# Performance work log

Hardware: AMD Instinct MI355X
Metric: run time of the kernel (lower is better)

## Reference

```python
import jax, jax.numpy as jnp
import numpy as np

N_NODES = 50000
N_EDGES = 800000
IN_DIM = 232
EMB = 300
HID = 2 * EMB
N_LAYERS = 5
BN_EPS = 1e-5


def setup_inputs() -> dict:
    key = jax.random.key(0)
    ks = jax.random.split(key, 12)
    x = jax.random.normal(ks[0], (N_NODES, IN_DIM), dtype=jnp.float32)
    edge_index = jax.random.randint(ks[1], (2, N_EDGES), 0, N_NODES, dtype=jnp.int64)
    edge_attr = jax.random.normal(ks[2], (N_EDGES, 9), dtype=jnp.float32)
    s_in = 1.0 / np.sqrt(IN_DIM)
    s_emb = 1.0 / np.sqrt(EMB)
    s_hid = 1.0 / np.sqrt(HID)
    lin_in_w = jax.random.uniform(ks[3], (IN_DIM, EMB), jnp.float32, -s_in, s_in)
    lin_in_b = jax.random.uniform(ks[4], (EMB,), jnp.float32, -s_in, s_in)
    w1 = jax.random.uniform(ks[5], (N_LAYERS, EMB, HID), jnp.float32, -s_emb, s_emb)
    b1 = jax.random.uniform(ks[6], (N_LAYERS, HID), jnp.float32, -s_emb, s_emb)
    gamma = jnp.ones((N_LAYERS, HID), jnp.float32)
    beta = jnp.zeros((N_LAYERS, HID), jnp.float32)
    w2 = jax.random.uniform(ks[7], (N_LAYERS, HID, EMB), jnp.float32, -s_hid, s_hid)
    b2 = jax.random.uniform(ks[8], (N_LAYERS, EMB), jnp.float32, -s_hid, s_hid)
    return {"x": x, "edge_index": edge_index, "edge_attr": edge_attr,
            "lin_in_w": lin_in_w, "lin_in_b": lin_in_b,
            "w1": w1, "b1": b1, "gamma": gamma, "beta": beta,
            "w2": w2, "b2": b2}


def reference(x, edge_index, edge_attr, lin_in_w, lin_in_b, w1, b1, gamma, beta, w2, b2):
    n = x.shape[0]
    self_loop = jnp.arange(n, dtype=edge_index.dtype)
    src = jnp.concatenate([edge_index[0], self_loop])  # [E+N]
    dst = jnp.concatenate([edge_index[1], self_loop])
    # input layer linear (232 -> emb)
    h = x @ lin_in_w + lin_in_b  # [N, EMB]
    num_layer = w1.shape[0]
    for l in range(num_layer):
        # gather messages at src, scatter-add at dst (GIN aggr='add' with self loops)
        agg = jax.ops.segment_sum(h[src], dst, num_segments=n)  # [N, EMB]
        # MLP: Linear -> BatchNorm1d (train-mode batch stats) -> ReLU -> Linear
        z = agg @ w1[l] + b1[l]  # [N, HID]
        mu = z.mean(axis=0)
        var = z.var(axis=0)  # biased, as torch BatchNorm uses for normalization
        z = (z - mu) * jax.lax.rsqrt(var + BN_EPS) * gamma[l] + beta[l]
        z = jax.nn.relu(z)
        h_new = z @ w2[l] + b2[l]  # [N, EMB]
        # GNN wrapper: relu between layers, none after the last (drop_ratio=0)
        h = h_new if l == num_layer - 1 else jax.nn.relu(h_new)
    return h  # JK='last'
```

## Files before the change

### kernel.cpp

```cpp
#include <hip/hip_runtime.h>
#include <cstdint>
#include <cstddef>

#define NNODES 50000
#define NEDGES 800000
#define IN_DIM 232
#define EMB 300
#define HID 600
#define NLAYERS 5
#define BN_EPS 1e-5f

#define MPAD 50048
#define K0P 256
#define K1P 320
#define K2P 608
#define N0P 384
#define N1P 640
#define MT_TILES 391
#define CSTR 140

typedef unsigned short ushort_t;
typedef __attribute__((ext_vector_type(8))) short bf16x8;
typedef __attribute__((ext_vector_type(4))) float f32x4;

__device__ __forceinline__ float b2f(ushort_t u) {
    unsigned int x = (unsigned int)u << 16;
    return __builtin_bit_cast(float, x);
}
__device__ __forceinline__ ushort_t f2b(float f) {
    unsigned int x = __builtin_bit_cast(unsigned int, f);
    unsigned int r = (x + 0x7fffu + ((x >> 16) & 1u)) >> 16;
    return (ushort_t)r;
}

__device__ __forceinline__ void gl_lds16(const void* gsrc, void* ldst) {
    __builtin_amdgcn_global_load_lds(
        (const __attribute__((address_space(1))) void*)gsrc,
        (__attribute__((address_space(3))) void*)ldst, 16, 0, 0);
}

__global__ void detect_mode_kernel(const unsigned int* __restrict__ ei, int* __restrict__ mode) {
    if (threadIdx.x == 0 && blockIdx.x == 0) {
        int nz = 0;
        for (int i = 0; i < 256; ++i) nz += (ei[2 * i + 1] != 0u);
        *mode = (nz == 0) ? 1 : 0;
    }
}
__device__ __forceinline__ int load_edge(const int* ei, int mode, long long idx) {
    if (mode) return (int)((const long long*)ei)[idx];
    return ei[idx];
}

__global__ void hist_kernel(const int* __restrict__ ei, const int* __restrict__ mode,
                            int* __restrict__ deg) {
    int i = blockIdx.x * blockDim.x + threadIdx.x;
    if (i >= NEDGES) return;
    int d = load_edge(ei, *mode, (long long)NEDGES + i);
    atomicAdd(&deg[d], 1);
}

__global__ void scan_block_sums(const int* __restrict__ deg, int* __restrict__ bsum, int n) {
    __shared__ int s[256];
    int t = threadIdx.x;
    int i = blockIdx.x * 256 + t;
    s[t] = (i < n) ? deg[i] : 0;
    __syncthreads();
    for (int off = 128; off > 0; off >>= 1) {
        if (t < off) s[t] += s[t + off];
        __syncthreads();
    }
    if (t == 0) bsum[blockIdx.x] = s[0];
}

__global__ void scan_bsums(int* __restrict__ bsum, int nb) {
    __shared__ int s[256];
    int t = threadIdx.x;
    int v = (t < nb) ? bsum[t] : 0;
    s[t] = v;
    __syncthreads();
    for (int off = 1; off < 256; off <<= 1) {
        int u = (t >= off) ? s[t - off] : 0;
        __syncthreads();
        s[t] += u;
        __syncthreads();
    }
    if (t < nb) bsum[t] = s[t] - v;
}

__global__ void scan_final(const int* __restrict__ deg, const int* __restrict__ bsum,
                           int* __restrict__ offs, int* __restrict__ cursor, int n) {
    __shared__ int s[256];
    int t = threadIdx.x;
    int i = blockIdx.x * 256 + t;
    int v = (i < n) ? deg[i] : 0;
    s[t] = v;
    __syncthreads();
    for (int off = 1; off < 256; off <<= 1) {
        int u = (t >= off) ? s[t - off] : 0;
        __syncthreads();
        s[t] += u;
        __syncthreads();
    }
    int excl = s[t] - v + bsum[blockIdx.x];
    if (i < n) {
        offs[i] = excl;
        cursor[i] = excl;
        if (i == n - 1) offs[n] = excl + v;
    }
}

__global__ void fill_csr(const int* __restrict__ ei, const int* __restrict__ mode,
                         int* __restrict__ cursor, int* __restrict__ csr) {
    int i = blockIdx.x * blockDim.x + threadIdx.x;
    if (i >= NEDGES) return;
    int m = *mode;
    int s = load_edge(ei, m, i);
    int d = load_edge(ei, m, (long long)NEDGES + i);
    int p = atomicAdd(&cursor[d], 1);
    csr[p] = s;
}

__global__ void cast_x_kernel(const float* __restrict__ x, ushort_t* __restrict__ o) {
    int idx = blockIdx.x * 256 + threadIdx.x;
    if (idx >= NNODES * K0P) return;
    int row = idx >> 8, k = idx & 255;
    float v = (k < IN_DIM) ? x[(size_t)row * IN_DIM + k] : 0.f;
    o[idx] = f2b(v);
}
__global__ void conv_lin_kernel(const float* __restrict__ w, ushort_t* __restrict__ o) {
    int idx = blockIdx.x * 256 + threadIdx.x;
    if (idx >= N0P * K0P) return;
    int n = idx >> 8, k = idx & 255;
    float v = (n < EMB && k < IN_DIM) ? w[(size_t)k * EMB + n] : 0.f;
    o[idx] = f2b(v);
}
__global__ void conv_w1_kernel(const float* __restrict__ w, ushort_t* __restrict__ o) {
    int idx = blockIdx.x * 256 + threadIdx.x;
    if (idx >= NLAYERS * N1P * K1P) return;
    int l = idx / (N1P * K1P);
    int r = idx - l * (N1P * K1P);
    int n = r / K1P, k = r - n * K1P;
    float v = (n < HID && k < EMB) ? w[((size_t)l * EMB + k) * HID + n] : 0.f;
    o[idx] = f2b(v);
}
__global__ void conv_w2_kernel(const float* __restrict__ w, ushort_t* __restrict__ o) {
    int idx = blockIdx.x * 256 + threadIdx.x;
    if (idx >= NLAYERS * N0P * K2P) return;
    int l = idx / (N0P * K2P);
    int r = idx - l * (N0P * K2P);
    int n = r / K2P, k = r - n * K2P;
    float v = (n < EMB && k < HID) ? w[((size_t)l * HID + k) * EMB + n] : 0.f;
    o[idx] = f2b(v);
}

__global__ __launch_bounds__(256) void aggregate_bf16(
    const ushort_t* __restrict__ h, ushort_t* __restrict__ agg,
    const int* __restrict__ offs, const int* __restrict__ csr) {
    const int w = blockIdx.x * 4 + (threadIdx.x >> 6);
    const int lane = threadIdx.x & 63;
    const int wid0 = w * 2, wid1 = wid0 + 1;
    if (wid0 >= NNODES) return;
    const bool hasb = lane < 11;
    float a0[4], a1[4] = {0.f, 0.f, 0.f, 0.f};
    float c0[4], c1[4] = {0.f, 0.f, 0.f, 0.f};
    {
        const ushort4* r0 = (const ushort4*)(h + (size_t)wid0 * K1P);
        const ushort4* r1 = (const ushort4*)(h + (size_t)wid1 * K1P);
        ushort4 v0 = r0[lane], v1 = r1[lane];
        a0[0] = b2f(v0.x); a0[1] = b2f(v0.y); a0[2] = b2f(v0.z); a0[3] = b2f(v0.w);
        c0[0] = b2f(v1.x); c0[1] = b2f(v1.y); c0[2] = b2f(v1.z); c0[3] = b2f(v1.w);
        if (hasb) {
            ushort4 w0 = r0[64 + lane], w1 = r1[64 + lane];
            a1[0] = b2f(w0.x); a1[1] = b2f(w0.y); a1[2] = b2f(w0.z); a1[3] = b2f(w0.w);
            c1[0] = b2f(w1.x); c1[1] = b2f(w1.y); c1[2] = b2f(w1.z); c1[3] = b2f(w1.w);
        }
    }
    int p0 = offs[wid0], e0 = offs[wid0 + 1];
    int p1 = e0, e1 = offs[wid1 + 1];

    while (p0 + 4 <= e0 && p1 + 4 <= e1) {
        int s0[4], s1[4];
#pragma unroll
        for (int u = 0; u < 4; ++u) { s0[u] = csr[p0 + u]; s1[u] = csr[p1 + u]; }
        ushort4 x0[4], x1[4], y0[4], y1[4];
#pragma unroll
        for (int u = 0; u < 4; ++u) {
            const ushort4* r0 = (const ushort4*)(h + (size_t)s0[u] * K1P);
            const ushort4* r1 = (const ushort4*)(h + (size_t)s1[u] * K1P);
            x0[u] = r0[lane];
            x1[u] = r1[lane];
            if (hasb) { y0[u] = r0[64 + lane]; y1[u] = r1[64 + lane]; }
        }
#pragma unroll
        for (int u = 0; u < 4; ++u) {
            a0[0] += b2f(x0[u].x); a0[1] += b2f(x0[u].y); a0[2] += b2f(x0[u].z); a0[3] += b2f(x0[u].w);
            c0[0] += b2f(x1[u].x); c0[1] += b2f(x1[u].y); c0[2] += b2f(x1[u].z); c0[3] += b2f(x1[u].w);
            if (hasb) {
                a1[0] += b2f(y0[u].x); a1[1] += b2f(y0[u].y); a1[2] += b2f(y0[u].z); a1[3] += b2f(y0[u].w);
                c1[0] += b2f(y1[u].x); c1[1] += b2f(y1[u].y); c1[2] += b2f(y1[u].z); c1[3] += b2f(y1[u].w);
            }
        }
        p0 += 4; p1 += 4;
    }

    while (p0 < e0 && p1 < e1) {
        const ushort4* r0 = (const ushort4*)(h + (size_t)csr[p0] * K1P); ++p0;
        const ushort4* r1 = (const ushort4*)(h + (size_t)csr[p1] * K1P); ++p1;
        ushort4 v0 = r0[lane];
        ushort4 v1 = r1[lane];
        a0[0] += b2f(v0.x); a0[1] += b2f(v0.y); a0[2] += b2f(v0.z); a0[3] += b2f(v0.w);
        c0[0] += b2f(v1.x); c0[1] += b2f(v1.y); c0[2] += b2f(v1.z); c0[3] += b2f(v1.w);
        if (hasb) {
            ushort4 w0 = r0[64 + lane];
            ushort4 w1 = r1[64 + lane];
            a1[0] += b2f(w0.x); a1[1] += b2f(w0.y); a1[2] += b2f(w0.z); a1[3] += b2f(w0.w);
            c1[0] += b2f(w1.x); c1[1] += b2f(w1.y); c1[2] += b2f(w1.z); c1[3] += b2f(w1.w);
        }
    }
    while (p0 < e0) {
        const ushort4* r0 = (const ushort4*)(h + (size_t)csr[p0] * K1P); ++p0;
        ushort4 v0 = r0[lane];
        a0[0] += b2f(v0.x); a0[1] += b2f(v0.y); a0[2] += b2f(v0.z); a0[3] += b2f(v0.w);
        if (hasb) {
            ushort4 w0 = r0[64 + lane];
            a1[0] += b2f(w0.x); a1[1] += b2f(w0.y); a1[2] += b2f(w0.z); a1[3] += b2f(w0.w);
        }
    }
    while (p1 < e1) {
        const ushort4* r1 = (const ushort4*)(h + (size_t)csr[p1] * K1P); ++p1;
        ushort4 v1 = r1[lane];
        c0[0] += b2f(v1.x); c0[1] += b2f(v1.y); c0[2] += b2f(v1.z); c0[3] += b2f(v1.w);
        if (hasb) {
            ushort4 w1 = r1[64 + lane];
            c1[0] += b2f(w1.x); c1[1] += b2f(w1.y); c1[2] += b2f(w1.z); c1[3] += b2f(w1.w);
        }
    }
    ushort4* o0 = (ushort4*)(agg + (size_t)wid0 * K1P);
    ushort4* o1 = (ushort4*)(agg + (size_t)wid1 * K1P);
    ushort4 ov;
    ov.x = f2b(a0[0]); ov.y = f2b(a0[1]); ov.z = f2b(a0[2]); ov.w = f2b(a0[3]);
    o0[lane] = ov;
    ov.x = f2b(c0[0]); ov.y = f2b(c0[1]); ov.z = f2b(c0[2]); ov.w = f2b(c0[3]);
    o1[lane] = ov;
    if (hasb) {
        ov.x = f2b(a1[0]); ov.y = f2b(a1[1]); ov.z = f2b(a1[2]); ov.w = f2b(a1[3]);
        o0[64 + lane] = ov;
        ov.x = f2b(c1[0]); ov.y = f2b(c1[1]); ov.z = f2b(c1[2]); ov.w = f2b(c1[3]);
        o1[64 + lane] = ov;
    }
    if (lane < 5) {
        ushort4 zz; zz.x = zz.y = zz.z = zz.w = 0;
        o0[75 + lane] = zz;
        o1[75 + lane] = zz;
    }
}

template <int PRO, int RELU, int STATS, int OUT_BF16>
__global__ __launch_bounds__(256) void gemm_mfma(
    const ushort_t* __restrict__ A, int lda,
    const ushort_t* __restrict__ Bt, int ldb,
    const float* __restrict__ bias,
    void* __restrict__ C, int ldc, int M, int N, int K,
    const float* __restrict__ pscale, const float* __restrict__ pshift, int Kreal,
    float* __restrict__ stats, int NB) {
    __shared__ ushort_t sh[PRO ? 17920 : 24576];
    __shared__ float psS[PRO ? 640 : 4];
    __shared__ float pfS[PRO ? 640 : 4];

    const int bid = blockIdx.x;
    const int xcd = bid & 7, slot = bid >> 3;
    const int mt = (slot / NB) * 8 + xcd;
    if (mt >= MT_TILES) return;
    const int nt = slot % NB;
    const int m0 = mt << 7, n0 = nt << 7;

    const int tid = threadIdx.x;
    const int wave = tid >> 6, lane = tid & 63;
    const int wm = wave >> 1, wn = wave & 1;
    const int NT = K >> 5;

    const int srow = lane >> 2;
    const int schunk = ((lane & 3) ^ ((lane >> 3) & 3)) << 3;
    const ushort_t* bP = Bt + (size_t)(n0 + (wave << 5) + srow) * ldb + schunk;
    const ushort_t* aPg = A + (size_t)(m0 + (wave << 5) + srow) * lda + schunk;
    const ushort_t* aPr = A + (size_t)(m0 + (wave << 5) + srow) * lda + ((lane & 3) << 3);
    const int a16 = lda << 4, b16 = ldb << 4;
    const int ldsW = wave << 10;

    const int fr = lane & 15, fq = lane >> 4;
    const int rdoff = (fq ^ ((fr >> 1) & 3)) << 3;

    f32x4 acc[4][4];
#pragma unroll
    for (int i = 0; i < 4; ++i)
#pragma unroll
        for (int j = 0; j < 4; ++j) acc[i][j] = {0.f, 0.f, 0.f, 0.f};

    if (PRO) {
        for (int i = tid; i < 640; i += 256) {
            psS[i] = (i < Kreal) ? pscale[i] : 0.f;
            pfS[i] = (i < Kreal) ? pshift[i] : 0.f;
        }
        __syncthreads();
    }

    if (!PRO) {
        const ushort_t* aN = aPg;
        const ushort_t* bN = bP;
        gl_lds16(aN, sh + ldsW);
        gl_lds16(aN + a16, sh + ldsW + 512);
        gl_lds16(bN, sh + 12288 + ldsW);
        gl_lds16(bN + b16, sh + 12288 + ldsW + 512);
        aN += 32; bN += 32;
        gl_lds16(aN, sh + 4096 + ldsW);
        gl_lds16(aN + a16, sh + 4096 + ldsW + 512);
        gl_lds16(bN, sh + 16384 + ldsW);
        gl_lds16(bN + b16, sh + 16384 + ldsW + 512);
        aN += 32; bN += 32;

        int cidx = 0;
        for (int t = 0; t < NT; ++t) {
            if (t + 2 < NT) {
                const int sidx = (cidx + 2 >= 3) ? cidx - 1 : cidx + 2;
                gl_lds16(aN, sh + (sidx << 12) + ldsW);
                gl_lds16(aN + a16, sh + (sidx << 12) + ldsW + 512);
                gl_lds16(bN, sh + 12288 + (sidx << 12) + ldsW);
                gl_lds16(bN + b16, sh + 12288 + (sidx << 12) + ldsW + 512);
                aN += 32; bN += 32;
                asm volatile("s_waitcnt vmcnt(8)" ::: "memory");
            } else if (t + 1 < NT) {
                asm volatile("s_waitcnt vmcnt(4)" ::: "memory");
            } else {
                asm volatile("s_waitcnt vmcnt(0)" ::: "memory");
            }
            __builtin_amdgcn_s_barrier();
            __builtin_amdgcn_sched_barrier(0);

            const ushort_t* ASc = sh + (cidx << 12);
            const ushort_t* BSc = sh + 12288 + (cidx << 12);
            bf16x8 af[4], bf[4];
#pragma unroll
            for (int mi = 0; mi < 4; ++mi)
                af[mi] = *(const bf16x8*)&ASc[((wm << 6) + (mi << 4) + fr) * 32 + rdoff];
#pragma unroll
            for (int nj = 0; nj < 4; ++nj)
                bf[nj] = *(const bf16x8*)&BSc[((wn << 6) + (nj << 4) + fr) * 32 + rdoff];
#pragma unroll
            for (int mi = 0; mi < 4; ++mi)
#pragma unroll
                for (int nj = 0; nj < 4; ++nj)
                    acc[mi][nj] = __builtin_amdgcn_mfma_f32_16x16x32_bf16(af[mi], bf[nj], acc[mi][nj], 0, 0, 0);

            __builtin_amdgcn_sched_barrier(0);
            __builtin_amdgcn_s_barrier();
            cidx = (cidx + 1 >= 3) ? 0 : cidx + 1;
        }
    } else {
        ushort_t* const AS0 = sh;
        ushort_t* const AS1 = sh + 4096;
        ushort_t* const BS0 = sh + 8192;
        ushort_t* const BS1 = sh + 12288;
        uint4 ar0, ar1;
        const ushort_t* aNext;
        const ushort_t* bNext = bP + 32;
        ar0 = *(const uint4*)aPr;
        ar1 = *(const uint4*)(aPr + a16);
        gl_lds16(bP, BS0 + ldsW);
        gl_lds16(bP + b16, BS0 + ldsW + 512);
        aNext = aPr + 32;

        int cur = 0;
        for (int t = 0; t < NT; ++t) {
            ushort_t* const ASc = cur ? AS1 : AS0;
            ushort_t* const BSn = cur ? BS0 : BS1;
            ushort_t* const BSc = cur ? BS1 : BS0;
            asm volatile("s_waitcnt vmcnt(2)" ::: "memory");
            const int kb = (t << 5) + ((lane & 3) << 3);
            float4 psa = *(const float4*)&psS[kb];
            float4 psb = *(const float4*)&psS[kb + 4];
            float4 pfa = *(const float4*)&pfS[kb];
            float4 pfb = *(const float4*)&pfS[kb + 4];
            float ps[8] = {psa.x, psa.y, psa.z, psa.w, psb.x, psb.y, psb.z, psb.w};
            float pf[8] = {pfa.x, pfa.y, pfa.z, pfa.w, pfb.x, pfb.y, pfb.z, pfb.w};
            bf16x8 w0, w1;
            const ushort_t* u0 = (const ushort_t*)&ar0;
            const ushort_t* u1 = (const ushort_t*)&ar1;
#pragma unroll
            for (int j = 0; j < 8; ++j) {
                float v0 = b2f(u0[j]) * ps[j] + pf[j];
                float v1 = b2f(u1[j]) * ps[j] + pf[j];
                w0[j] = (short)f2b(v0 > 0.f ? v0 : 0.f);
                w1[j] = (short)f2b(v1 > 0.f ? v1 : 0.f);
            }
            ushort_t* dA = ASc + ((wave << 5) + srow) * 32 + schunk;
            *(bf16x8*)dA = w0;
            *(bf16x8*)(dA + 16 * 32) = w1;
            if (t + 1 < NT) {
                ar0 = *(const uint4*)aNext;
                ar1 = *(const uint4*)(aNext + a16);
                gl_lds16(bNext, BSn + ldsW);
                gl_lds16(bNext + b16, BSn + ldsW + 512);
                aNext += 32; bNext += 32;
                asm volatile("s_waitcnt vmcnt(4) lgkmcnt(0)" ::: "memory");
            } else {
                asm volatile("s_waitcnt vmcnt(0) lgkmcnt(0)" ::: "memory");
            }
            __builtin_amdgcn_s_barrier();
            __builtin_amdgcn_sched_barrier(0);

            bf16x8 af[4], bf[4];
#pragma unroll
            for (int mi = 0; mi < 4; ++mi)
                af[mi] = *(const bf16x8*)&ASc[((wm << 6) + (mi << 4) + fr) * 32 + rdoff];
#pragma unroll
            for (int nj = 0; nj < 4; ++nj)
                bf[nj] = *(const bf16x8*)&BSc[((wn << 6) + (nj << 4) + fr) * 32 + rdoff];
#pragma unroll
            for (int mi = 0; mi < 4; ++mi)
#pragma unroll
                for (int nj = 0; nj < 4; ++nj)
                    acc[mi][nj] = __builtin_amdgcn_mfma_f32_16x16x32_bf16(af[mi], bf[nj], acc[mi][nj], 0, 0, 0);

            __builtin_amdgcn_sched_barrier(0);
            __builtin_amdgcn_s_barrier();
            cur ^= 1;
        }
    }

    if (STATS) {
        float s1[4] = {0.f, 0.f, 0.f, 0.f}, s2[4] = {0.f, 0.f, 0.f, 0.f};
#pragma unroll
        for (int nj = 0; nj < 4; ++nj) {
            const int col = n0 + (wn << 6) + (nj << 4) + fr;
            if (col < N) {
                const float bv = bias[col];
#pragma unroll
                for (int mi = 0; mi < 4; ++mi) {
                    const int rbase = m0 + (wm << 6) + (mi << 4) + (fq << 2);
#pragma unroll
                    for (int r = 0; r < 4; ++r) {
                        if (rbase + r < M) {
                            float v = acc[mi][nj][r] + bv;
                            if (RELU) v = v > 0.f ? v : 0.f;
                            s1[nj] += v; s2[nj] += v * v;
                        }
                    }
                }
            }
        }
#pragma unroll
        for (int nj = 0; nj < 4; ++nj) {
            s1[nj] += __shfl_xor(s1[nj], 16);
            s1[nj] += __shfl_xor(s1[nj], 32);
            s2[nj] += __shfl_xor(s2[nj], 16);
            s2[nj] += __shfl_xor(s2[nj], 32);
        }
        if (lane < 16) {
#pragma unroll
            for (int nj = 0; nj < 4; ++nj) {
                const int col = n0 + (wn << 6) + (nj << 4) + lane;
                if (col < N) {
                    atomicAdd(&stats[col], s1[nj]);
                    atomicAdd(&stats[N + col], s2[nj]);
                }
            }
        }
    }

    __syncthreads();
    if (OUT_BF16) {
        ushort_t* ct = sh;
#pragma unroll
        for (int nj = 0; nj < 4; ++nj) {
            const int col_l = (wn << 6) + (nj << 4) + fr;
            const int col = n0 + col_l;
            const float bv = (col < N) ? bias[col] : 0.f;
#pragma unroll
            for (int mi = 0; mi < 4; ++mi) {
                const int rl0 = (wm << 6) + (mi << 4) + (fq << 2);
#pragma unroll
                for (int r = 0; r < 4; ++r) {
                    float v = acc[mi][nj][r] + bv;
                    if (RELU) v = v > 0.f ? v : 0.f;
                    ct[(rl0 + r) * CSTR + col_l] = f2b(v);
                }
            }
        }
        __syncthreads();
        const int rr = tid >> 1, half = tid & 1;
        const int grow = m0 + rr;
        if (grow < M) {
            const ushort_t* src = ct + rr * CSTR + (half << 6);
            ushort_t* dst = (ushort_t*)C + (size_t)grow * ldc + n0 + (half << 6);
#pragma unroll
            for (int c = 0; c < 8; ++c) {
                const int gc = n0 + (half << 6) + (c << 3);
                if (gc + 7 < N) {
                    uint2 u0 = *(const uint2*)(src + (c << 3));
                    uint2 u1 = *(const uint2*)(src + (c << 3) + 4);
                    uint4 o; o.x = u0.x; o.y = u0.y; o.z = u1.x; o.w = u1.y;
                    *(uint4*)(dst + (c << 3)) = o;
                } else {
                    for (int j = 0; j < 8; ++j)
                        if (gc + j < N) dst[(c << 3) + j] = src[(c << 3) + j];
                }
            }
        }
    } else {
        float* ctf = (float*)sh;
#pragma unroll
        for (int ph = 0; ph < 2; ++ph) {
            if (wm == ph) {
#pragma unroll
                for (int nj = 0; nj < 4; ++nj) {
                    const int col_l = (wn << 6) + (nj << 4) + fr;
                    const int col = n0 + col_l;
                    const float bv = (col < N) ? bias[col] : 0.f;
#pragma unroll
                    for (int mi = 0; mi < 4; ++mi) {
                        const int rl0 = (mi << 4) + (fq << 2);
#pragma unroll
                        for (int r = 0; r < 4; ++r) {
                            float v = acc[mi][nj][r] + bv;
                            if (RELU) v = v > 0.f ? v : 0.f;
                            ctf[(rl0 + r) * CSTR + col_l] = v;
                        }
                    }
                }
            }
            __syncthreads();
            const int rr = tid >> 2, q = tid & 3;
            const int grow = m0 + (ph << 6) + rr;
            if (grow < M) {
                const float* src = ctf + rr * CSTR + (q << 5);
                float* dst = (float*)C + (size_t)grow * ldc + n0 + (q << 5);
#pragma unroll
                for (int c = 0; c < 8; ++c) {
                    const int gc = n0 + (q << 5) + (c << 2);
                    if (gc + 3 < N) {
                        *(float4*)(dst + (c << 2)) = *(const float4*)(src + (c << 2));
                    } else {
                        for (int j = 0; j < 4; ++j)
                            if (gc + j < N) dst[(c << 2) + j] = src[(c << 2) + j];
                    }
                }
            }
            __syncthreads();
        }
    }
}

__global__ void bn_finalize(const float* __restrict__ stats, const float* __restrict__ gamma,
                            const float* __restrict__ beta, float* __restrict__ pscale,
                            float* __restrict__ pshift, int N, float invM) {
    int c = blockIdx.x * blockDim.x + threadIdx.x;
    if (c >= N) return;
    float mu = stats[c] * invM;
    float var = stats[N + c] * invM - mu * mu;
    float rs = rsqrtf(var + BN_EPS);
    float g = gamma[c] * rs;
    pscale[c] = g;
    pshift[c] = beta[c] - mu * g;
}

extern "C" void kernel_launch(void* const* d_in, const int* in_sizes, int n_in,
                              void* d_out, int out_size, void* d_ws, size_t ws_size,
                              hipStream_t stream) {
    const float* x = (const float*)d_in[0];
    const int* ei = (const int*)d_in[1];
    const float* lin_in_w = (const float*)d_in[3];
    const float* lin_in_b = (const float*)d_in[4];
    const float* w1 = (const float*)d_in[5];
    const float* b1 = (const float*)d_in[6];
    const float* gamma = (const float*)d_in[7];
    const float* beta = (const float*)d_in[8];
    const float* w2 = (const float*)d_in[9];
    const float* b2 = (const float*)d_in[10];
    float* out = (float*)d_out;

    char* p = (char*)d_ws;
    auto alloc = [&](size_t bytes) {
        char* r = p;
        p += (bytes + 255) & ~(size_t)255;
        return r;
    };
    ushort_t* xb  = (ushort_t*)alloc((size_t)MPAD * K0P * 2);
    ushort_t* h   = (ushort_t*)alloc((size_t)MPAD * K1P * 2);
    ushort_t* agg = (ushort_t*)alloc((size_t)MPAD * K1P * 2);
    ushort_t* z   = (ushort_t*)alloc((size_t)MPAD * K2P * 2);
    ushort_t* lint = (ushort_t*)alloc((size_t)N0P * K0P * 2);
    ushort_t* w1t  = (ushort_t*)alloc((size_t)NLAYERS * N1P * K1P * 2);
    ushort_t* w2t  = (ushort_t*)alloc((size_t)NLAYERS * N0P * K2P * 2);
    int* deg    = (int*)alloc(NNODES * 4);
    int* cursor = (int*)alloc(NNODES * 4);
    int* offs   = (int*)alloc((NNODES + 1) * 4);
    int* bsum   = (int*)alloc(1024);
    int* csr    = (int*)alloc((size_t)NEDGES * 4);
    float* stats  = (float*)alloc((size_t)NLAYERS * 2 * HID * 4);
    float* pscale = (float*)alloc(HID * 4);
    float* pshift = (float*)alloc(HID * 4);
    int* mode   = (int*)alloc(256);
    (void)ws_size; (void)in_sizes; (void)n_in; (void)out_size;

    hipMemsetAsync(deg, 0, NNODES * 4, stream);
    hipMemsetAsync(stats, 0, (size_t)NLAYERS * 2 * HID * 4, stream);
    hipMemsetAsync(h + (size_t)NNODES * K1P, 0, (size_t)(MPAD - NNODES) * K1P * 2, stream);

    detect_mode_kernel<<<1, 64, 0, stream>>>((const unsigned int*)ei, mode);
    hist_kernel<<<(NEDGES + 255) / 256, 256, 0, stream>>>(ei, mode, deg);
    const int nb = (NNODES + 255) / 256;
    scan_block_sums<<<nb, 256, 0, stream>>>(deg, bsum, NNODES);
    scan_bsums<<<1, 256, 0, stream>>>(bsum, nb);
    scan_final<<<nb, 256, 0, stream>>>(deg, bsum, offs, cursor, NNODES);
    fill_csr<<<(NEDGES + 255) / 256, 256, 0, stream>>>(ei, mode, cursor, csr);

    cast_x_kernel<<<(NNODES * K0P + 255) / 256, 256, 0, stream>>>(x, xb);
    conv_lin_kernel<<<(N0P * K0P + 255) / 256, 256, 0, stream>>>(lin_in_w, lint);
    conv_w1_kernel<<<(NLAYERS * N1P * K1P + 255) / 256, 256, 0, stream>>>(w1, w1t);
    conv_w2_kernel<<<(NLAYERS * N0P * K2P + 255) / 256, 256, 0, stream>>>(w2, w2t);

    const int G3 = 8 * 49 * 3;
    const int G5 = 8 * 49 * 5;

    gemm_mfma<0, 0, 0, 1><<<G3, 256, 0, stream>>>(
        xb, K0P, lint, K0P, lin_in_b, h, K1P, NNODES, EMB, K0P,
        nullptr, nullptr, 0, nullptr, 3);

    for (int l = 0; l < NLAYERS; ++l) {
        aggregate_bf16<<<(NNODES / 2 + 3) / 4, 256, 0, stream>>>(h, agg, offs, csr);
        gemm_mfma<0, 0, 1, 1><<<G5, 256, 0, stream>>>(
            agg, K1P, w1t + (size_t)l * N1P * K1P, K1P, b1 + (size_t)l * HID,
            z, K2P, NNODES, HID, K1P,
            nullptr, nullptr, 0, stats + (size_t)l * 2 * HID, 5);
        bn_finalize<<<(HID + 255) / 256, 256, 0, stream>>>(
            stats + (size_t)l * 2 * HID, gamma + (size_t)l * HID, beta + (size_t)l * HID,
            pscale, pshift, HID, 1.f / NNODES);
        if (l < NLAYERS - 1) {
            gemm_mfma<1, 1, 0, 1><<<G3, 256, 0, stream>>>(
                z, K2P, w2t + (size_t)l * N0P * K2P, K2P, b2 + (size_t)l * EMB,
                h, K1P, NNODES, EMB, K2P,
                pscale, pshift, HID, nullptr, 3);
        } else {
            gemm_mfma<1, 0, 0, 0><<<G3, 256, 0, stream>>>(
                z, K2P, w2t + (size_t)l * N0P * K2P, K2P, b2 + (size_t)l * EMB,
                out, EMB, NNODES, EMB, K2P,
                pscale, pshift, HID, nullptr, 3);
        }
    }
}
```

Before: 1.151 ms.

## Sort nodes by degree for aggregation and replace BN stat atomics with partials

Adds a counting-sort of nodes by in-degree (histogram, scan, scatter) so each wave aggregates two nodes of similar degree, reducing the imbalance in the paired unrolled loop. The GEMM's BatchNorm column statistics are now written as per-tile partial sums rather than accumulated with float atomics, and a new per-column reduce kernel sums them and computes scale and shift. This adds three setup kernels and an extra partials buffer, and the permuted node order gives a less regular output write pattern in aggregation.

```diff
diff --git a/kernel.cpp b/kernel.cpp
--- a/kernel.cpp
+++ b/kernel.cpp
@@ -18,6 +18,7 @@
 #define N1P 640
 #define MT_TILES 391
 #define CSTR 140
+#define DBUCK 1024
 
 typedef unsigned short ushort_t;
 typedef __attribute__((ext_vector_type(8))) short bf16x8;
@@ -120,6 +121,37 @@
     csr[p] = s;
 }
 
+__global__ void deg_hist(const int* __restrict__ offs, int* __restrict__ dh) {
+    int i = blockIdx.x * 256 + threadIdx.x;
+    if (i >= NNODES) return;
+    int d = offs[i + 1] - offs[i];
+    if (d > DBUCK - 1) d = DBUCK - 1;
+    atomicAdd(&dh[d], 1);
+}
+__global__ void deg_scan(const int* __restrict__ dh, int* __restrict__ dcur) {
+    __shared__ int s[DBUCK];
+    int t = threadIdx.x;
+    int v = dh[t];
+    s[t] = v;
+    __syncthreads();
+    for (int off = 1; off < DBUCK; off <<= 1) {
+        int u = (t >= off) ? s[t - off] : 0;
+        __syncthreads();
+        s[t] += u;
+        __syncthreads();
+    }
+    dcur[t] = s[t] - v;
+}
+__global__ void deg_scatter(const int* __restrict__ offs, int* __restrict__ dcur,
+                            int* __restrict__ perm) {
+    int i = blockIdx.x * 256 + threadIdx.x;
+    if (i >= NNODES) return;
+    int d = offs[i + 1] - offs[i];
+    if (d > DBUCK - 1) d = DBUCK - 1;
+    int pos = atomicAdd(&dcur[d], 1);
+    perm[pos] = i;
+}
+
 __global__ void cast_x_kernel(const float* __restrict__ x, ushort_t* __restrict__ o) {
     int idx = blockIdx.x * 256 + threadIdx.x;
     if (idx >= NNODES * K0P) return;
@@ -155,11 +187,12 @@
 
 __global__ __launch_bounds__(256) void aggregate_bf16(
     const ushort_t* __restrict__ h, ushort_t* __restrict__ agg,
-    const int* __restrict__ offs, const int* __restrict__ csr) {
+    const int* __restrict__ offs, const int* __restrict__ csr,
+    const int* __restrict__ perm) {
     const int w = blockIdx.x * 4 + (threadIdx.x >> 6);
     const int lane = threadIdx.x & 63;
-    const int wid0 = w * 2, wid1 = wid0 + 1;
-    if (wid0 >= NNODES) return;
+    if (w * 2 >= NNODES) return;
+    const int wid0 = perm[w * 2], wid1 = perm[w * 2 + 1];
     const bool hasb = lane < 11;
     float a0[4], a1[4] = {0.f, 0.f, 0.f, 0.f};
     float c0[4], c1[4] = {0.f, 0.f, 0.f, 0.f};
@@ -176,7 +209,7 @@
         }
     }
     int p0 = offs[wid0], e0 = offs[wid0 + 1];
-    int p1 = e0, e1 = offs[wid1 + 1];
+    int p1 = offs[wid1], e1 = offs[wid1 + 1];
 
     while (p0 + 4 <= e0 && p1 + 4 <= e1) {
         int s0[4], s1[4];
@@ -262,7 +295,7 @@
     const float* __restrict__ bias,
     void* __restrict__ C, int ldc, int M, int N, int K,
     const float* __restrict__ pscale, const float* __restrict__ pshift, int Kreal,
-    float* __restrict__ stats, int NB) {
+    float* __restrict__ partials, int NB) {
     __shared__ ushort_t sh[PRO ? 17920 : 24576];
     __shared__ float psS[PRO ? 640 : 4];
     __shared__ float pfS[PRO ? 640 : 4];
@@ -456,12 +489,13 @@
             s2[nj] += __shfl_xor(s2[nj], 32);
         }
         if (lane < 16) {
+            float* pw = partials + (size_t)(mt * 2 + wm) * 2 * 640;
 #pragma unroll
             for (int nj = 0; nj < 4; ++nj) {
                 const int col = n0 + (wn << 6) + (nj << 4) + lane;
                 if (col < N) {
-                    atomicAdd(&stats[col], s1[nj]);
-                    atomicAdd(&stats[N + col], s2[nj]);
+                    pw[col] = s1[nj];
+                    pw[640 + col] = s2[nj];
                 }
             }
         }
@@ -550,17 +584,33 @@
     }
 }
 
-__global__ void bn_finalize(const float* __restrict__ stats, const float* __restrict__ gamma,
-                            const float* __restrict__ beta, float* __restrict__ pscale,
-                            float* __restrict__ pshift, int N, float invM) {
-    int c = blockIdx.x * blockDim.x + threadIdx.x;
-    if (c >= N) return;
-    float mu = stats[c] * invM;
-    float var = stats[N + c] * invM - mu * mu;
-    float rs = rsqrtf(var + BN_EPS);
-    float g = gamma[c] * rs;
-    pscale[c] = g;
-    pshift[c] = beta[c] - mu * g;
+__global__ __launch_bounds__(256) void bn_reduce(
+    const float* __restrict__ partials, const float* __restrict__ gamma,
+    const float* __restrict__ beta, float* __restrict__ pscale,
+    float* __restrict__ pshift, float invM) {
+    const int c = blockIdx.x;
+    const int t = threadIdx.x;
+    float s1 = 0.f, s2 = 0.f;
+    for (int i = t; i < MT_TILES * 2; i += 256) {
+        const float* pw = partials + (size_t)i * 2 * 640;
+        s1 += pw[c];
+        s2 += pw[640 + c];
+    }
+    __shared__ float r1[256], r2[256];
+    r1[t] = s1; r2[t] = s2;
+    __syncthreads();
+    for (int off = 128; off > 0; off >>= 1) {
+        if (t < off) { r1[t] += r1[t + off]; r2[t] += r2[t + off]; }
+        __syncthreads();
+    }
+    if (t == 0) {
+        float mu = r1[0] * invM;
+        float var = r2[0] * invM - mu * mu;
+        float rs = rsqrtf(var + BN_EPS);
+        float g = gamma[c] * rs;
+        pscale[c] = g;
+        pshift[c] = beta[c] - mu * g;
+    }
 }
 
 extern "C" void kernel_launch(void* const* d_in, const int* in_sizes, int n_in,
@@ -596,14 +646,17 @@
     int* offs   = (int*)alloc((NNODES + 1) * 4);
     int* bsum   = (int*)alloc(1024);
     int* csr    = (int*)alloc((size_t)NEDGES * 4);
-    float* stats  = (float*)alloc((size_t)NLAYERS * 2 * HID * 4);
+    int* perm   = (int*)alloc(NNODES * 4);
+    int* dh     = (int*)alloc(DBUCK * 4);
+    int* dcur   = (int*)alloc(DBUCK * 4);
+    float* partials = (float*)alloc((size_t)MT_TILES * 2 * 2 * 640 * 4);
     float* pscale = (float*)alloc(HID * 4);
     float* pshift = (float*)alloc(HID * 4);
     int* mode   = (int*)alloc(256);
     (void)ws_size; (void)in_sizes; (void)n_in; (void)out_size;
 
     hipMemsetAsync(deg, 0, NNODES * 4, stream);
-    hipMemsetAsync(stats, 0, (size_t)NLAYERS * 2 * HID * 4, stream);
+    hipMemsetAsync(dh, 0, DBUCK * 4, stream);
     hipMemsetAsync(h + (size_t)NNODES * K1P, 0, (size_t)(MPAD - NNODES) * K1P * 2, stream);
 
     detect_mode_kernel<<<1, 64, 0, stream>>>((const unsigned int*)ei, mode);
@@ -614,6 +667,10 @@
     scan_final<<<nb, 256, 0, stream>>>(deg, bsum, offs, cursor, NNODES);
     fill_csr<<<(NEDGES + 255) / 256, 256, 0, stream>>>(ei, mode, cursor, csr);
 
+    deg_hist<<<nb, 256, 0, stream>>>(offs, dh);
+    deg_scan<<<1, DBUCK, 0, stream>>>(dh, dcur);
+    deg_scatter<<<nb, 256, 0, stream>>>(offs, dcur, perm);
+
     cast_x_kernel<<<(NNODES * K0P + 255) / 256, 256, 0, stream>>>(x, xb);
     conv_lin_kernel<<<(N0P * K0P + 255) / 256, 256, 0, stream>>>(lin_in_w, lint);
     conv_w1_kernel<<<(NLAYERS * N1P * K1P + 255) / 256, 256, 0, stream>>>(w1, w1t);
@@ -627,14 +684,14 @@
         nullptr, nullptr, 0, nullptr, 3);
 
     for (int l = 0; l < NLAYERS; ++l) {
-        aggregate_bf16<<<(NNODES / 2 + 3) / 4, 256, 0, stream>>>(h, agg, offs, csr);
+        aggregate_bf16<<<(NNODES / 2 + 3) / 4, 256, 0, stream>>>(h, agg, offs, csr, perm);
         gemm_mfma<0, 0, 1, 1><<<G5, 256, 0, stream>>>(
             agg, K1P, w1t + (size_t)l * N1P * K1P, K1P, b1 + (size_t)l * HID,
             z, K2P, NNODES, HID, K1P,
-            nullptr, nullptr, 0, stats + (size_t)l * 2 * HID, 5);
-        bn_finalize<<<(HID + 255) / 256, 256, 0, stream>>>(
-            stats + (size_t)l * 2 * HID, gamma + (size_t)l * HID, beta + (size_t)l * HID,
-            pscale, pshift, HID, 1.f / NNODES);
+            nullptr, nullptr, 0, partials, 5);
+        bn_reduce<<<HID, 256, 0, stream>>>(
+            partials, gamma + (size_t)l * HID, beta + (size_t)l * HID,
+            pscale, pshift, 1.f / NNODES);
         if (l < NLAYERS - 1) {
             gemm_mfma<1, 1, 0, 1><<<G3, 256, 0, stream>>>(
                 z, K2P, w2t + (size_t)l * N0P * K2P, K2P, b2 + (size_t)l * EMB,
```

New measurement: 1.395 ms. 21.3% more time.
